# Performance work log

Hardware: AMD Instinct MI355X
Metric: run time of the kernel (lower is better)

## Reference

```python
import jax, jax.numpy as jnp
import numpy as np

N_NODES = 32768
N_EDGES = 524288
HID = 128


def _linear_params(key, fan_in, fan_out):
    kw, kb = jax.random.split(key)
    bound = 1.0 / np.sqrt(fan_in)
    w = jax.random.uniform(kw, (fan_in, fan_out), jnp.float32, -bound, bound)
    b = jax.random.uniform(kb, (fan_out,), jnp.float32, -bound, bound)
    return w, b


def setup_inputs() -> dict:
    key = jax.random.key(0)
    ks = jax.random.split(key, 8)
    x = jax.random.normal(ks[0], (N_NODES, HID), jnp.float32)
    edge_attr = jax.random.normal(ks[1], (N_EDGES, HID), jnp.float32)
    edges = jax.random.randint(ks[2], (2, N_EDGES), 0, N_NODES, jnp.int32)
    w1, b1 = _linear_params(ks[3], 3 * HID, HID)      # message_fn layer 1
    w2, b2 = _linear_params(ks[4], HID, HID)          # message_fn layer 2
    wu1, bu1 = _linear_params(ks[5], HID, 2 * HID)    # update_fn layer 1
    wu2, bu2 = _linear_params(ks[6], 2 * HID, HID)    # update_fn layer 2
    return {"x": x, "edge_attr": edge_attr, "edges": edges,
            "w1": w1, "b1": b1, "w2": w2, "b2": b2,
            "wu1": wu1, "bu1": bu1, "wu2": wu2, "bu2": bu2}


def reference(x, edge_attr, edges, w1, b1, w2, b2, wu1, bu1, wu2, bu2):
    n_nodes = x.shape[0]
    send, recv = edges[0], edges[1]
    # gather endpoint features and concat with edge attributes: [E, 3*HID]
    ea = jnp.concatenate([x[send], x[recv], edge_attr], axis=-1)
    # per-edge message MLP (Linear-SiLU-Linear-SiLU)
    h = jax.nn.silu(ea @ w1 + b1)
    msg = jax.nn.silu(h @ w2 + b2)                    # [E, HID]
    # scatter-mean into receiving nodes
    sums = jax.ops.segment_sum(msg, recv, num_segments=n_nodes)
    counts = jax.ops.segment_sum(jnp.ones((msg.shape[0],), msg.dtype), recv,
                                 num_segments=n_nodes)
    aggr = sums / jnp.maximum(counts, 1.0)[:, None]
    # residual (input_size == hidden_size -> Identity) + update MLP
    xo = x + aggr
    xo = xo + (jax.nn.silu(xo @ wu1 + bu1) @ wu2 + bu2)
    return xo, msg
```

## Files before the change

### kernel.cpp

```cpp
#include <hip/hip_runtime.h>
#include <hip/hip_bf16.h>

#define NN 32768
#define NE 524288
#define HID 128

typedef unsigned short u16;
typedef unsigned int u32;
typedef __bf16 bf16x8 __attribute__((ext_vector_type(8)));
typedef float f32x4 __attribute__((ext_vector_type(4)));

__device__ __forceinline__ u16 f2bf(float f) {
  return __builtin_bit_cast(u16, (__bf16)f);
}
__device__ __forceinline__ float silu_f(float v) {
  return v * __builtin_amdgcn_rcpf(1.f + __expf(-v));
}
__device__ __forceinline__ bf16x8 cvt8(float4 a, float4 b) {
  bf16x8 r;
  r[0] = (__bf16)a.x; r[1] = (__bf16)a.y; r[2] = (__bf16)a.z; r[3] = (__bf16)a.w;
  r[4] = (__bf16)b.x; r[5] = (__bf16)b.y; r[6] = (__bf16)b.z; r[7] = (__bf16)b.w;
  return r;
}
__device__ __forceinline__ float4 f4fma(float4 x, float4 s, float inv) {
  return make_float4(x.x + s.x * inv, x.y + s.y * inv,
                     x.z + s.z * inv, x.w + s.w * inv);
}

__device__ __forceinline__ void gld16(const void* g, void* l) {
  __builtin_amdgcn_global_load_lds(
      (const __attribute__((address_space(1))) u32*)g,
      (__attribute__((address_space(3))) u32*)l, 16, 0, 0);
}

#define WV(N)  do { asm volatile("s_waitcnt vmcnt(" #N ")" ::: "memory"); \
                    __builtin_amdgcn_sched_barrier(0); } while (0)
#define WVL(N) do { asm volatile("s_waitcnt vmcnt(" #N ") lgkmcnt(0)" ::: "memory"); \
                    __builtin_amdgcn_sched_barrier(0); } while (0)
#define WL()   do { asm volatile("s_waitcnt lgkmcnt(0)" ::: "memory"); \
                    __builtin_amdgcn_sched_barrier(0); } while (0)
__device__ __forceinline__ void bar() {
  __builtin_amdgcn_sched_barrier(0);
  __builtin_amdgcn_s_barrier();
  __builtin_amdgcn_sched_barrier(0);
}

__global__ __launch_bounds__(256) void prep_k(
    const float* __restrict__ x, const float* __restrict__ w1,
    const float* __restrict__ w2, const float* __restrict__ wu1,
    const float* __restrict__ wu2, const int* __restrict__ recv,
    u16* __restrict__ xb, u16* __restrict__ w1Ts, u16* __restrict__ w2Ts,
    u16* __restrict__ wu1T, u16* __restrict__ wu2T, int* __restrict__ cnt)
{
  int i = blockIdx.x * 256 + threadIdx.x;
  xb[i] = f2bf(x[i]);
  if (i < NE) atomicAdd(&cnt[recv[i]], 1);
  if (i < 3 * 128 * 128) {
    int j = i & 7, qs = (i >> 3) & 15, c = (i >> 7) & 127, s = i >> 14;
    int k = s * 128 + ((qs ^ (c & 7)) << 3) + j;
    w1Ts[i] = f2bf(w1[k * 128 + c]);
  }
  if (i < 128 * 128) {
    int j = i & 7, qs = (i >> 3) & 15, c = i >> 7;
    int k = ((qs ^ (c & 7)) << 3) + j;
    w2Ts[i] = f2bf(w2[k * 128 + c]);
  }
  if (i < 256 * 128) { int c = i >> 7, k = i & 127; wu1T[i] = f2bf(wu1[k * 256 + c]); }
  if (i < 128 * 256) { int c = i >> 8, k = i & 255; wu2T[i] = f2bf(wu2[k * 128 + c]); }
}

__global__ __launch_bounds__(1024) void scan_k(const int* __restrict__ cnt,
                                               int* __restrict__ cursor)
{
  __shared__ int part[1024];
  const int tid = threadIdx.x;
  const int base = tid * 32;
  int v[32];
  int s = 0;
  #pragma unroll
  for (int j = 0; j < 32; ++j) { v[j] = cnt[base + j]; s += v[j]; }
  part[tid] = s;
  __syncthreads();
  #pragma unroll 1
  for (int d = 1; d < 1024; d <<= 1) {
    int t = (tid >= d) ? part[tid - d] : 0;
    __syncthreads();
    part[tid] += t;
    __syncthreads();
  }
  int ex = part[tid] - s;
  #pragma unroll
  for (int j = 0; j < 32; ++j) {
    cursor[base + j] = ex;
    ex += v[j];
  }
}

__global__ __launch_bounds__(256) void scatter_k(const int* __restrict__ recv,
                                                 int* __restrict__ cursor,
                                                 int* __restrict__ eperm)
{
  int e = blockIdx.x * 256 + threadIdx.x;
  int r = recv[e];
  int pos = atomicAdd(&cursor[r], 1);
  eperm[pos] = e;
}

__global__ __launch_bounds__(512, 4) void edge_mlp(
    const u16* __restrict__ xb, const float* __restrict__ eattr,
    const int* __restrict__ send, const int* __restrict__ recv,
    const int* __restrict__ eperm,
    const u16* __restrict__ w1Ts, const float* __restrict__ b1,
    const u16* __restrict__ w2Ts, const float* __restrict__ b2,
    float* __restrict__ msg_out, float* __restrict__ sums)
{
  __shared__ u16 sA[128 * 128];
  __shared__ u16 sB[128 * 128];
  __shared__ int sNid[128];

  const int tid  = threadIdx.x;
  const int lane = tid & 63;
  const int w    = tid >> 6;
  const int wr   = w >> 1;
  const int wc   = w & 1;
  const int fr   = lane & 15;
  const int fkq  = lane >> 4;
  const int orow = fkq * 4;
  const int lrow4 = lane >> 4;
  const int schk  = lane & 15;
  const int logical = ((int)blockIdx.x & 7) * ((int)gridDim.x >> 3)
                    + ((int)blockIdx.x >> 3);
  const int e0 = logical * 128;

  int eo[4], ns[4], nr[4], rl[4];
  #pragma unroll
  for (int i = 0; i < 4; ++i) {
    rl[i] = w * 16 + i * 4 + lrow4;
    eo[i] = eperm[e0 + rl[i]];
  }
  #pragma unroll
  for (int i = 0; i < 4; ++i) {
    ns[i] = send[eo[i]];
    nr[i] = recv[eo[i]];
    if (schk == 0) sNid[rl[i]] = nr[i];
  }

  f32x4 acc[2][4];
  #pragma unroll
  for (int m = 0; m < 2; ++m)
    #pragma unroll
    for (int n = 0; n < 4; ++n)
      #pragma unroll
      for (int r = 0; r < 4; ++r) acc[m][n][r] = 0.f;

  #pragma unroll
  for (int i = 0; i < 4; ++i)
    gld16(xb + ((size_t)ns[i] << 7) + ((schk ^ (rl[i] & 7)) << 3),
          sA + ((w * 16 + i * 4) << 7));
  #pragma unroll
  for (int i = 0; i < 4; ++i)
    gld16(w1Ts + ((w * 16 + i * 4) << 7) + (lane << 3),
          sB + ((w * 16 + i * 4) << 7));
  __builtin_amdgcn_sched_barrier(0);
  float4 ea0[4], ea1[4];
  #pragma unroll
  for (int i = 0; i < 4; ++i) {
    const float* ep = eattr + ((size_t)eo[i] << 7) + ((schk ^ (rl[i] & 7)) << 3);
    ea0[i] = *reinterpret_cast<const float4*>(ep);
    ea1[i] = *reinterpret_cast<const float4*>(ep + 4);
  }
  __builtin_amdgcn_sched_barrier(0);

  auto cslice = [&](const u16* bufA) {
    #pragma unroll
    for (int kk = 0; kk < 4; ++kk) {
      bf16x8 aF[2], bF[4];
      #pragma unroll
      for (int m = 0; m < 2; ++m) {
        int row = wr * 32 + m * 16 + fr;
        int ch = (kk * 4 + fkq) ^ (row & 7);
        aF[m] = __builtin_bit_cast(bf16x8,
            *reinterpret_cast<const uint4*>(bufA + (row << 7) + (ch << 3)));
      }
      #pragma unroll
      for (int n = 0; n < 4; ++n) {
        int c = wc * 64 + n * 16 + fr;
        int ch = (kk * 4 + fkq) ^ (c & 7);
        bF[n] = __builtin_bit_cast(bf16x8,
            *reinterpret_cast<const uint4*>(sB + (c << 7) + (ch << 3)));
      }
      __builtin_amdgcn_s_setprio(1);
      #pragma unroll
      for (int m = 0; m < 2; ++m)
        #pragma unroll
        for (int n = 0; n < 4; ++n)
          acc[m][n] = __builtin_amdgcn_mfma_f32_16x16x32_bf16(aF[m], bF[n], acc[m][n], 0, 0, 0);
      __builtin_amdgcn_s_setprio(0);
    }
  };

  WV(8); bar();
  float b1v[4], b2v[4];
  #pragma unroll
  for (int n = 0; n < 4; ++n) {
    b1v[n] = b1[wc * 64 + n * 16 + fr];
    b2v[n] = b2[wc * 64 + n * 16 + fr];
  }
  cslice(sA);
  bar();
  #pragma unroll
  for (int i = 0; i < 4; ++i)
    gld16(xb + ((size_t)nr[i] << 7) + ((schk ^ (rl[i] & 7)) << 3),
          sA + ((w * 16 + i * 4) << 7));
  #pragma unroll
  for (int i = 0; i < 4; ++i)
    gld16(w1Ts + 16384 + ((w * 16 + i * 4) << 7) + (lane << 3),
          sB + ((w * 16 + i * 4) << 7));
  WV(0); bar();
  cslice(sA);
  bar();
  #pragma unroll
  for (int i = 0; i < 4; ++i)
    *reinterpret_cast<uint4*>(sA + (rl[i] << 7) + (schk << 3)) =
        __builtin_bit_cast(uint4, cvt8(ea0[i], ea1[i]));
  #pragma unroll
  for (int i = 0; i < 4; ++i)
    gld16(w1Ts + 32768 + ((w * 16 + i * 4) << 7) + (lane << 3),
          sB + ((w * 16 + i * 4) << 7));
  WVL(0); bar();
  cslice(sA);
  bar();
  #pragma unroll
  for (int i = 0; i < 4; ++i)
    gld16(w2Ts + ((w * 16 + i * 4) << 7) + (lane << 3),
          sB + ((w * 16 + i * 4) << 7));
  #pragma unroll
  for (int n = 0; n < 4; ++n) {
    int c = wc * 64 + n * 16 + fr;
    #pragma unroll
    for (int m = 0; m < 2; ++m)
      #pragma unroll
      for (int r = 0; r < 4; ++r) {
        int row = wr * 32 + m * 16 + orow + r;
        sA[(row << 7) + (((c >> 3) ^ (row & 7)) << 3) + (c & 7)] =
            f2bf(silu_f(acc[m][n][r] + b1v[n]));
        acc[m][n][r] = 0.f;
      }
  }
  WVL(0); bar();
  cslice(sA);

  int eg0[4], eg1[4];
  #pragma unroll
  for (int r = 0; r < 4; ++r) {
    eg0[r] = eperm[e0 + wr * 32 + orow + r];
    eg1[r] = eperm[e0 + wr * 32 + 16 + orow + r];
  }
  bar();

  #pragma unroll
  for (int m = 0; m < 2; ++m)
    #pragma unroll
    for (int r = 0; r < 4; ++r) {
      int row = wr * 32 + m * 16 + orow + r;
      float* mp = msg_out + ((size_t)(m ? eg1[r] : eg0[r]) << 7);
      #pragma unroll
      for (int n = 0; n < 4; ++n) {
        int c = wc * 64 + n * 16 + fr;
        float v = silu_f(acc[m][n][r] + b2v[n]);
        mp[c] = v;
        sA[(row << 7) + (((c >> 3) ^ (row & 7)) << 3) + (c & 7)] = f2bf(v);
      }
    }
  WL(); bar();

  {
    const int col = tid & 127, q = tid >> 7;
    float s = 0.f;
    int cur = sNid[q * 32];
    #pragma unroll 1
    for (int r = 0; r < 32; ++r) {
      int row = q * 32 + r;
      u16 hv = sA[(row << 7) + (((col >> 3) ^ (row & 7)) << 3) + (col & 7)];
      s += __builtin_bit_cast(float, (u32)hv << 16);
      int nxt = (r < 31) ? sNid[row + 1] : -1;
      if (nxt != cur) {
        atomicAdd(sums + (size_t)cur * HID + col, s);
        s = 0.f;
        cur = nxt;
      }
    }
  }
}

__global__ __launch_bounds__(256) void mlp1_k(
    const float* __restrict__ x, const float* __restrict__ sums,
    const int* __restrict__ cnt, const u16* __restrict__ wu1T,
    const float* __restrict__ bu1, u16* __restrict__ t)
{
  __shared__ u16 sB[256][40];
  const int tid = threadIdx.x, lane = tid & 63, wid = tid >> 6;
  const int wr = wid >> 1, wc = wid & 1;
  const int fr = lane & 15, fkq = lane >> 4, fk = fkq * 8, orow = fkq * 4;
  const int n0 = blockIdx.x * 64;

  float invm[2];
  #pragma unroll
  for (int m = 0; m < 2; ++m)
    invm[m] = __builtin_amdgcn_rcpf(fmaxf((float)cnt[n0 + wr * 32 + m * 16 + fr], 1.f));

  f32x4 acc[2][8];
  #pragma unroll
  for (int m = 0; m < 2; ++m)
    #pragma unroll
    for (int n = 0; n < 8; ++n)
      #pragma unroll
      for (int r = 0; r < 4; ++r) acc[m][n][r] = 0.f;

  #pragma unroll 1
  for (int kk = 0; kk < 4; ++kk) {
    #pragma unroll
    for (int it = 0; it < 4; ++it) {
      int chunk = tid + it * 256;
      int c = chunk >> 2, q = chunk & 3;
      *reinterpret_cast<uint4*>(&sB[c][q * 8]) =
          *reinterpret_cast<const uint4*>(wu1T + c * 128 + kk * 32 + q * 8);
    }
    __syncthreads();
    bf16x8 aF[2], bF[8];
    #pragma unroll
    for (int m = 0; m < 2; ++m) {
      size_t base = (size_t)(n0 + wr * 32 + m * 16 + fr) * HID + kk * 32 + fk;
      float4 xv0 = *reinterpret_cast<const float4*>(x + base);
      float4 xv1 = *reinterpret_cast<const float4*>(x + base + 4);
      float4 sv0 = *reinterpret_cast<const float4*>(sums + base);
      float4 sv1 = *reinterpret_cast<const float4*>(sums + base + 4);
      aF[m] = cvt8(f4fma(xv0, sv0, invm[m]), f4fma(xv1, sv1, invm[m]));
    }
    #pragma unroll
    for (int n = 0; n < 8; ++n)
      bF[n] = __builtin_bit_cast(bf16x8,
          *reinterpret_cast<const uint4*>(&sB[wc * 128 + n * 16 + fr][fk]));
    #pragma unroll
    for (int m = 0; m < 2; ++m)
      #pragma unroll
      for (int n = 0; n < 8; ++n)
        acc[m][n] = __builtin_amdgcn_mfma_f32_16x16x32_bf16(aF[m], bF[n], acc[m][n], 0, 0, 0);
    __syncthreads();
  }
  #pragma unroll
  for (int n = 0; n < 8; ++n) {
    int col = wc * 128 + n * 16 + fr;
    float bb = bu1[col];
    #pragma unroll
    for (int m = 0; m < 2; ++m) {
      int row = n0 + wr * 32 + m * 16 + orow;
      #pragma unroll
      for (int r = 0; r < 4; ++r)
        t[(size_t)(row + r) * 256 + col] = f2bf(silu_f(acc[m][n][r] + bb));
    }
  }
}

__global__ __launch_bounds__(256) void mlp2_k(
    const u16* __restrict__ t, const u16* __restrict__ wu2T,
    const float* __restrict__ bu2, const float* __restrict__ x,
    const float* __restrict__ sums, const int* __restrict__ cnt,
    float* __restrict__ xo)
{
  __shared__ u16 sB[128][40];
  const int tid = threadIdx.x, lane = tid & 63, wid = tid >> 6;
  const int wr = wid >> 1, wc = wid & 1;
  const int fr = lane & 15, fk = (lane >> 4) * 8, orow = (lane >> 4) * 4;
  const int n0 = blockIdx.x * 64;

  f32x4 acc[2][4];
  #pragma unroll
  for (int m = 0; m < 2; ++m)
    #pragma unroll
    for (int n = 0; n < 4; ++n)
      #pragma unroll
      for (int r = 0; r < 4; ++r) acc[m][n][r] = 0.f;

  #pragma unroll 1
  for (int kk = 0; kk < 8; ++kk) {
    #pragma unroll
    for (int it = 0; it < 2; ++it) {
      int chunk = tid + it * 256;
      int c = chunk >> 2, q = chunk & 3;
      *reinterpret_cast<uint4*>(&sB[c][q * 8]) =
          *reinterpret_cast<const uint4*>(wu2T + c * 256 + kk * 32 + q * 8);
    }
    __syncthreads();
    bf16x8 aF[2], bF[4];
    #pragma unroll
    for (int m = 0; m < 2; ++m)
      aF[m] = __builtin_bit_cast(bf16x8, *reinterpret_cast<const uint4*>(
          t + (size_t)(n0 + wr * 32 + m * 16 + fr) * 256 + kk * 32 + fk));
    #pragma unroll
    for (int n = 0; n < 4; ++n)
      bF[n] = __builtin_bit_cast(bf16x8,
          *reinterpret_cast<const uint4*>(&sB[wc * 64 + n * 16 + fr][fk]));
    #pragma unroll
    for (int m = 0; m < 2; ++m)
      #pragma unroll
      for (int n = 0; n < 4; ++n)
        acc[m][n] = __builtin_amdgcn_mfma_f32_16x16x32_bf16(aF[m], bF[n], acc[m][n], 0, 0, 0);
    __syncthreads();
  }
  #pragma unroll
  for (int m = 0; m < 2; ++m) {
    #pragma unroll
    for (int r = 0; r < 4; ++r) {
      int gn = n0 + wr * 32 + m * 16 + orow + r;
      float inv = 1.f / fmaxf((float)cnt[gn], 1.f);
      #pragma unroll
      for (int n = 0; n < 4; ++n) {
        int col = wc * 64 + n * 16 + fr;
        float xi = x[(size_t)gn * HID + col] + sums[(size_t)gn * HID + col] * inv;
        xo[(size_t)gn * HID + col] = xi + acc[m][n][r] + bu2[col];
      }
    }
  }
}

extern "C" void kernel_launch(void* const* d_in, const int* in_sizes, int n_in,
                              void* d_out, int out_size, void* d_ws, size_t ws_size,
                              hipStream_t stream)
{
  (void)in_sizes; (void)n_in; (void)out_size; (void)ws_size;
  const float* x     = (const float*)d_in[0];
  const float* eattr = (const float*)d_in[1];
  const int*   edges = (const int*)d_in[2];
  const float* w1  = (const float*)d_in[3];
  const float* b1  = (const float*)d_in[4];
  const float* w2  = (const float*)d_in[5];
  const float* b2  = (const float*)d_in[6];
  const float* wu1 = (const float*)d_in[7];
  const float* bu1 = (const float*)d_in[8];
  const float* wu2 = (const float*)d_in[9];
  const float* bu2 = (const float*)d_in[10];

  float* xo  = (float*)d_out;
  float* msg = xo + (size_t)NN * HID;

  char* p = (char*)d_ws;
  u16* xb    = (u16*)p; p += (size_t)NN * HID * 2;
  u16* w1Ts  = (u16*)p; p += 384 * 128 * 2;
  u16* w2Ts  = (u16*)p; p += 128 * 128 * 2;
  u16* wu1T  = (u16*)p; p += 256 * 128 * 2;
  u16* wu2T  = (u16*)p; p += 128 * 256 * 2;
  u16* tbuf  = (u16*)p; p += (size_t)NN * 256 * 2;
  float* sums = (float*)p; p += (size_t)NN * HID * 4;
  int* cnt    = (int*)p; p += (size_t)NN * 4;
  int* cursor = (int*)p; p += (size_t)NN * 4;
  int* eperm  = (int*)p; p += (size_t)NE * 4;

  const int* send = edges;
  const int* recv = edges + NE;

  hipMemsetAsync(cnt, 0, (size_t)NN * 4, stream);
  hipMemsetAsync(sums, 0, (size_t)NN * HID * 4, stream);
  prep_k<<<NN * HID / 256, 256, 0, stream>>>(x, w1, w2, wu1, wu2, recv,
                                             xb, w1Ts, w2Ts, wu1T, wu2T, cnt);
  scan_k<<<1, 1024, 0, stream>>>(cnt, cursor);
  scatter_k<<<NE / 256, 256, 0, stream>>>(recv, cursor, eperm);
  edge_mlp<<<NE / 128, 512, 0, stream>>>(xb, eattr, send, recv, eperm,
                                         w1Ts, b1, w2Ts, b2, msg, sums);
  mlp1_k<<<NN / 64, 256, 0, stream>>>(x, sums, cnt, wu1T, bu1, tbuf);
  mlp2_k<<<NN / 64, 256, 0, stream>>>(tbuf, wu2T, bu2, x, sums, cnt, xo);
}
```

Before: 324.5 us.

## Halve edge tile to 64 rows with separate sender/receiver LDS buffers

Shrinks the edge_mlp tile from 128 to 64 edges per block and rearranges the 8 waves as 2x4 over the output tile, with each wave computing a 32x32 slice. Sender and receiver node gathers go into two separate LDS buffers, so both are issued up front instead of the receiver gather waiting until after the first K-slice. This is meant to lower LDS use and register pressure, raising occupancy, and to overlap the gather latency. In exchange the full weight tiles are loaded into LDS twice as often in total and the block count doubles.

```diff
diff --git a/kernel.cpp b/kernel.cpp
--- a/kernel.cpp
+++ b/kernel.cpp
@@ -34,8 +34,6 @@
 }
 
 #define WV(N)  do { asm volatile("s_waitcnt vmcnt(" #N ")" ::: "memory"); \
-                    __builtin_amdgcn_sched_barrier(0); } while (0)
-#define WVL(N) do { asm volatile("s_waitcnt vmcnt(" #N ") lgkmcnt(0)" ::: "memory"); \
                     __builtin_amdgcn_sched_barrier(0); } while (0)
 #define WL()   do { asm volatile("s_waitcnt lgkmcnt(0)" ::: "memory"); \
                     __builtin_amdgcn_sched_barrier(0); } while (0)
@@ -114,15 +112,16 @@
     const u16* __restrict__ w2Ts, const float* __restrict__ b2,
     float* __restrict__ msg_out, float* __restrict__ sums)
 {
-  __shared__ u16 sA[128 * 128];
-  __shared__ u16 sB[128 * 128];
-  __shared__ int sNid[128];
+  __shared__ u16 sA0[64 * 128];
+  __shared__ u16 sA1[64 * 128];
+  __shared__ u16 sB[128 * 128 / 2 * 2];
+  __shared__ int sNid[64];
 
   const int tid  = threadIdx.x;
   const int lane = tid & 63;
   const int w    = tid >> 6;
-  const int wr   = w >> 1;
-  const int wc   = w & 1;
+  const int wr   = w >> 2;
+  const int wc   = w & 3;
   const int fr   = lane & 15;
   const int fkq  = lane >> 4;
   const int orow = fkq * 4;
@@ -130,51 +129,63 @@
   const int schk  = lane & 15;
   const int logical = ((int)blockIdx.x & 7) * ((int)gridDim.x >> 3)
                     + ((int)blockIdx.x >> 3);
-  const int e0 = logical * 128;
-
-  int eo[4], ns[4], nr[4], rl[4];
-  #pragma unroll
-  for (int i = 0; i < 4; ++i) {
-    rl[i] = w * 16 + i * 4 + lrow4;
+  const int e0 = logical * 64;
+
+  int eo[2], ns[2], nr[2], rl[2];
+  #pragma unroll
+  for (int i = 0; i < 2; ++i) {
+    rl[i] = w * 8 + i * 4 + lrow4;
     eo[i] = eperm[e0 + rl[i]];
   }
   #pragma unroll
-  for (int i = 0; i < 4; ++i) {
+  for (int i = 0; i < 2; ++i) {
     ns[i] = send[eo[i]];
     nr[i] = recv[eo[i]];
     if (schk == 0) sNid[rl[i]] = nr[i];
   }
 
-  f32x4 acc[2][4];
-  #pragma unroll
-  for (int m = 0; m < 2; ++m)
-    #pragma unroll
-    for (int n = 0; n < 4; ++n)
+  f32x4 acc[2][2];
+  #pragma unroll
+  for (int m = 0; m < 2; ++m)
+    #pragma unroll
+    for (int n = 0; n < 2; ++n)
       #pragma unroll
       for (int r = 0; r < 4; ++r) acc[m][n][r] = 0.f;
 
-  #pragma unroll
-  for (int i = 0; i < 4; ++i)
+  float b1v[2], b2v[2];
+  #pragma unroll
+  for (int n = 0; n < 2; ++n) {
+    b1v[n] = b1[wc * 32 + n * 16 + fr];
+    b2v[n] = b2[wc * 32 + n * 16 + fr];
+  }
+  __builtin_amdgcn_sched_barrier(0);
+  #pragma unroll
+  for (int i = 0; i < 2; ++i)
     gld16(xb + ((size_t)ns[i] << 7) + ((schk ^ (rl[i] & 7)) << 3),
-          sA + ((w * 16 + i * 4) << 7));
+          sA0 + ((w * 8 + i * 4) << 7));
   #pragma unroll
   for (int i = 0; i < 4; ++i)
     gld16(w1Ts + ((w * 16 + i * 4) << 7) + (lane << 3),
           sB + ((w * 16 + i * 4) << 7));
   __builtin_amdgcn_sched_barrier(0);
-  float4 ea0[4], ea1[4];
-  #pragma unroll
-  for (int i = 0; i < 4; ++i) {
+  #pragma unroll
+  for (int i = 0; i < 2; ++i)
+    gld16(xb + ((size_t)nr[i] << 7) + ((schk ^ (rl[i] & 7)) << 3),
+          sA1 + ((w * 8 + i * 4) << 7));
+  __builtin_amdgcn_sched_barrier(0);
+  float4 ea[2][2];
+  #pragma unroll
+  for (int i = 0; i < 2; ++i) {
     const float* ep = eattr + ((size_t)eo[i] << 7) + ((schk ^ (rl[i] & 7)) << 3);
-    ea0[i] = *reinterpret_cast<const float4*>(ep);
-    ea1[i] = *reinterpret_cast<const float4*>(ep + 4);
+    ea[i][0] = *reinterpret_cast<const float4*>(ep);
+    ea[i][1] = *reinterpret_cast<const float4*>(ep + 4);
   }
   __builtin_amdgcn_sched_barrier(0);
 
   auto cslice = [&](const u16* bufA) {
     #pragma unroll
     for (int kk = 0; kk < 4; ++kk) {
-      bf16x8 aF[2], bF[4];
+      bf16x8 aF[2], bF[2];
       #pragma unroll
       for (int m = 0; m < 2; ++m) {
         int row = wr * 32 + m * 16 + fr;
@@ -183,8 +194,8 @@
             *reinterpret_cast<const uint4*>(bufA + (row << 7) + (ch << 3)));
       }
       #pragma unroll
-      for (int n = 0; n < 4; ++n) {
-        int c = wc * 64 + n * 16 + fr;
+      for (int n = 0; n < 2; ++n) {
+        int c = wc * 32 + n * 16 + fr;
         int ch = (kk * 4 + fkq) ^ (c & 7);
         bF[n] = __builtin_bit_cast(bf16x8,
             *reinterpret_cast<const uint4*>(sB + (c << 7) + (ch << 3)));
@@ -193,69 +204,58 @@
       #pragma unroll
       for (int m = 0; m < 2; ++m)
         #pragma unroll
-        for (int n = 0; n < 4; ++n)
+        for (int n = 0; n < 2; ++n)
           acc[m][n] = __builtin_amdgcn_mfma_f32_16x16x32_bf16(aF[m], bF[n], acc[m][n], 0, 0, 0);
       __builtin_amdgcn_s_setprio(0);
     }
   };
 
-  WV(8); bar();
-  float b1v[4], b2v[4];
-  #pragma unroll
-  for (int n = 0; n < 4; ++n) {
-    b1v[n] = b1[wc * 64 + n * 16 + fr];
-    b2v[n] = b2[wc * 64 + n * 16 + fr];
-  }
-  cslice(sA);
+  WV(6); bar();
+  cslice(sA0);
   bar();
-  #pragma unroll
-  for (int i = 0; i < 4; ++i)
-    gld16(xb + ((size_t)nr[i] << 7) + ((schk ^ (rl[i] & 7)) << 3),
-          sA + ((w * 16 + i * 4) << 7));
   #pragma unroll
   for (int i = 0; i < 4; ++i)
     gld16(w1Ts + 16384 + ((w * 16 + i * 4) << 7) + (lane << 3),
           sB + ((w * 16 + i * 4) << 7));
   WV(0); bar();
-  cslice(sA);
+  cslice(sA1);
   bar();
   #pragma unroll
-  for (int i = 0; i < 4; ++i)
-    *reinterpret_cast<uint4*>(sA + (rl[i] << 7) + (schk << 3)) =
-        __builtin_bit_cast(uint4, cvt8(ea0[i], ea1[i]));
+  for (int i = 0; i < 2; ++i)
+    *reinterpret_cast<uint4*>(sA0 + (rl[i] << 7) + (schk << 3)) =
+        __builtin_bit_cast(uint4, cvt8(ea[i][0], ea[i][1]));
   #pragma unroll
   for (int i = 0; i < 4; ++i)
     gld16(w1Ts + 32768 + ((w * 16 + i * 4) << 7) + (lane << 3),
           sB + ((w * 16 + i * 4) << 7));
-  WVL(0); bar();
-  cslice(sA);
+  WV(0); WL(); bar();
+  cslice(sA0);
   bar();
   #pragma unroll
   for (int i = 0; i < 4; ++i)
     gld16(w2Ts + ((w * 16 + i * 4) << 7) + (lane << 3),
           sB + ((w * 16 + i * 4) << 7));
   #pragma unroll
-  for (int n = 0; n < 4; ++n) {
-    int c = wc * 64 + n * 16 + fr;
-    #pragma unroll
-    for (int m = 0; m < 2; ++m)
+  for (int m = 0; m < 2; ++m)
+    #pragma unroll
+    for (int n = 0; n < 2; ++n) {
+      int c = wc * 32 + n * 16 + fr;
       #pragma unroll
       for (int r = 0; r < 4; ++r) {
         int row = wr * 32 + m * 16 + orow + r;
-        sA[(row << 7) + (((c >> 3) ^ (row & 7)) << 3) + (c & 7)] =
+        sA1[(row << 7) + (((c >> 3) ^ (row & 7)) << 3) + (c & 7)] =
             f2bf(silu_f(acc[m][n][r] + b1v[n]));
         acc[m][n][r] = 0.f;
       }
-  }
-  WVL(0); bar();
-  cslice(sA);
-
-  int eg0[4], eg1[4];
-  #pragma unroll
-  for (int r = 0; r < 4; ++r) {
-    eg0[r] = eperm[e0 + wr * 32 + orow + r];
-    eg1[r] = eperm[e0 + wr * 32 + 16 + orow + r];
-  }
+    }
+  WV(0); WL(); bar();
+  int eg[2][4];
+  #pragma unroll
+  for (int m = 0; m < 2; ++m)
+    #pragma unroll
+    for (int r = 0; r < 4; ++r)
+      eg[m][r] = eperm[e0 + wr * 32 + m * 16 + orow + r];
+  cslice(sA1);
   bar();
 
   #pragma unroll
@@ -263,13 +263,13 @@
     #pragma unroll
     for (int r = 0; r < 4; ++r) {
       int row = wr * 32 + m * 16 + orow + r;
-      float* mp = msg_out + ((size_t)(m ? eg1[r] : eg0[r]) << 7);
-      #pragma unroll
-      for (int n = 0; n < 4; ++n) {
-        int c = wc * 64 + n * 16 + fr;
+      float* mp = msg_out + ((size_t)eg[m][r] << 7);
+      #pragma unroll
+      for (int n = 0; n < 2; ++n) {
+        int c = wc * 32 + n * 16 + fr;
         float v = silu_f(acc[m][n][r] + b2v[n]);
         mp[c] = v;
-        sA[(row << 7) + (((c >> 3) ^ (row & 7)) << 3) + (c & 7)] = f2bf(v);
+        sA0[(row << 7) + (((c >> 3) ^ (row & 7)) << 3) + (c & 7)] = f2bf(v);
       }
     }
   WL(); bar();
@@ -277,13 +277,13 @@
   {
     const int col = tid & 127, q = tid >> 7;
     float s = 0.f;
-    int cur = sNid[q * 32];
+    int cur = sNid[q * 16];
     #pragma unroll 1
-    for (int r = 0; r < 32; ++r) {
-      int row = q * 32 + r;
-      u16 hv = sA[(row << 7) + (((col >> 3) ^ (row & 7)) << 3) + (col & 7)];
+    for (int r = 0; r < 16; ++r) {
+      int row = q * 16 + r;
+      u16 hv = sA0[(row << 7) + (((col >> 3) ^ (row & 7)) << 3) + (col & 7)];
       s += __builtin_bit_cast(float, (u32)hv << 16);
-      int nxt = (r < 31) ? sNid[row + 1] : -1;
+      int nxt = (r < 15) ? sNid[row + 1] : -1;
       if (nxt != cur) {
         atomicAdd(sums + (size_t)cur * HID + col, s);
         s = 0.f;
@@ -465,8 +465,8 @@
                                              xb, w1Ts, w2Ts, wu1T, wu2T, cnt);
   scan_k<<<1, 1024, 0, stream>>>(cnt, cursor);
   scatter_k<<<NE / 256, 256, 0, stream>>>(recv, cursor, eperm);
-  edge_mlp<<<NE / 128, 512, 0, stream>>>(xb, eattr, send, recv, eperm,
-                                         w1Ts, b1, w2Ts, b2, msg, sums);
+  edge_mlp<<<NE / 64, 512, 0, stream>>>(xb, eattr, send, recv, eperm,
+                                        w1Ts, b1, w2Ts, b2, msg, sums);
   mlp1_k<<<NN / 64, 256, 0, stream>>>(x, sums, cnt, wu1T, bu1, tbuf);
   mlp2_k<<<NN / 64, 256, 0, stream>>>(tbuf, wu2T, bu2, x, sums, cnt, xo);
 }
```

Result: no change. 327.1 us (+0.8%).

## Halve edge-MLP weight LDS staging, pre-permute endpoint ids, vectorize x conversion

Applied to the files above, without the earlier changes.

The edge MLP now stages each 128-column weight panel into shared memory as two 64-column halves. This cuts LDS use so the launch bound can rise to 6 blocks per CU, at the cost of twice as many barrier-separated stage and compute steps. The scatter kernel now also writes sender and receiver ids in sorted order, so the edge MLP no longer makes dependent indirect loads through eperm to fetch them. The edge-attribute prefetch is moved later and loses its overlap with the first GEMM slices. Separately, prep_k converts x to bf16 four floats per thread, so it launches a quarter as many blocks.

```diff
diff --git a/kernel.cpp b/kernel.cpp
--- a/kernel.cpp
+++ b/kernel.cpp
@@ -12,6 +12,9 @@
 
 __device__ __forceinline__ u16 f2bf(float f) {
   return __builtin_bit_cast(u16, (__bf16)f);
+}
+__device__ __forceinline__ float bf2f(u16 h) {
+  return __builtin_bit_cast(float, (u32)h << 16);
 }
 __device__ __forceinline__ float silu_f(float v) {
   return v * __builtin_amdgcn_rcpf(1.f + __expf(-v));
@@ -34,8 +37,6 @@
 }
 
 #define WV(N)  do { asm volatile("s_waitcnt vmcnt(" #N ")" ::: "memory"); \
-                    __builtin_amdgcn_sched_barrier(0); } while (0)
-#define WVL(N) do { asm volatile("s_waitcnt vmcnt(" #N ") lgkmcnt(0)" ::: "memory"); \
                     __builtin_amdgcn_sched_barrier(0); } while (0)
 #define WL()   do { asm volatile("s_waitcnt lgkmcnt(0)" ::: "memory"); \
                     __builtin_amdgcn_sched_barrier(0); } while (0)
@@ -53,7 +54,11 @@
     u16* __restrict__ wu1T, u16* __restrict__ wu2T, int* __restrict__ cnt)
 {
   int i = blockIdx.x * 256 + threadIdx.x;
-  xb[i] = f2bf(x[i]);
+  float4 xv = reinterpret_cast<const float4*>(x)[i];
+  uint2 pv;
+  pv.x = (u32)f2bf(xv.x) | ((u32)f2bf(xv.y) << 16);
+  pv.y = (u32)f2bf(xv.z) | ((u32)f2bf(xv.w) << 16);
+  reinterpret_cast<uint2*>(xb)[i] = pv;
   if (i < NE) atomicAdd(&cnt[recv[i]], 1);
   if (i < 3 * 128 * 128) {
     int j = i & 7, qs = (i >> 3) & 15, c = (i >> 7) & 127, s = i >> 14;
@@ -96,26 +101,32 @@
   }
 }
 
-__global__ __launch_bounds__(256) void scatter_k(const int* __restrict__ recv,
+__global__ __launch_bounds__(256) void scatter_k(const int* __restrict__ send,
+                                                 const int* __restrict__ recv,
                                                  int* __restrict__ cursor,
-                                                 int* __restrict__ eperm)
+                                                 int* __restrict__ eperm,
+                                                 int* __restrict__ sid,
+                                                 int* __restrict__ rid)
 {
   int e = blockIdx.x * 256 + threadIdx.x;
   int r = recv[e];
+  int s = send[e];
   int pos = atomicAdd(&cursor[r], 1);
   eperm[pos] = e;
-}
-
-__global__ __launch_bounds__(512, 4) void edge_mlp(
+  sid[pos] = s;
+  rid[pos] = r;
+}
+
+__global__ __launch_bounds__(512, 6) void edge_mlp(
     const u16* __restrict__ xb, const float* __restrict__ eattr,
-    const int* __restrict__ send, const int* __restrict__ recv,
-    const int* __restrict__ eperm,
-    const u16* __restrict__ w1Ts, const float* __restrict__ b1,
-    const u16* __restrict__ w2Ts, const float* __restrict__ b2,
+    const int* __restrict__ eperm, const int* __restrict__ sid,
+    const int* __restrict__ rid,
+    const u16* __restrict__ wTs, const float* __restrict__ b1,
+    const float* __restrict__ b2,
     float* __restrict__ msg_out, float* __restrict__ sums)
 {
   __shared__ u16 sA[128 * 128];
-  __shared__ u16 sB[128 * 128];
+  __shared__ u16 sB[64 * 128];
   __shared__ int sNid[128];
 
   const int tid  = threadIdx.x;
@@ -137,125 +148,128 @@
   for (int i = 0; i < 4; ++i) {
     rl[i] = w * 16 + i * 4 + lrow4;
     eo[i] = eperm[e0 + rl[i]];
-  }
-  #pragma unroll
-  for (int i = 0; i < 4; ++i) {
-    ns[i] = send[eo[i]];
-    nr[i] = recv[eo[i]];
+    ns[i] = sid[e0 + rl[i]];
+    nr[i] = rid[e0 + rl[i]];
+  }
+  #pragma unroll
+  for (int i = 0; i < 4; ++i)
     if (schk == 0) sNid[rl[i]] = nr[i];
-  }
-
-  f32x4 acc[2][4];
-  #pragma unroll
-  for (int m = 0; m < 2; ++m)
-    #pragma unroll
-    for (int n = 0; n < 4; ++n)
-      #pragma unroll
-      for (int r = 0; r < 4; ++r) acc[m][n][r] = 0.f;
-
-  #pragma unroll
-  for (int i = 0; i < 4; ++i)
-    gld16(xb + ((size_t)ns[i] << 7) + ((schk ^ (rl[i] & 7)) << 3),
-          sA + ((w * 16 + i * 4) << 7));
-  #pragma unroll
-  for (int i = 0; i < 4; ++i)
-    gld16(w1Ts + ((w * 16 + i * 4) << 7) + (lane << 3),
-          sB + ((w * 16 + i * 4) << 7));
-  __builtin_amdgcn_sched_barrier(0);
-  float4 ea0[4], ea1[4];
-  #pragma unroll
-  for (int i = 0; i < 4; ++i) {
-    const float* ep = eattr + ((size_t)eo[i] << 7) + ((schk ^ (rl[i] & 7)) << 3);
-    ea0[i] = *reinterpret_cast<const float4*>(ep);
-    ea1[i] = *reinterpret_cast<const float4*>(ep + 4);
-  }
-  __builtin_amdgcn_sched_barrier(0);
-
-  auto cslice = [&](const u16* bufA) {
+
+  float b1v[2][2], b2v[2][2];
+  #pragma unroll
+  for (int h = 0; h < 2; ++h)
+    #pragma unroll
+    for (int n = 0; n < 2; ++n) {
+      int c = h * 64 + wc * 32 + n * 16 + fr;
+      b1v[h][n] = b1[c];
+      b2v[h][n] = b2[c];
+    }
+
+  f32x4 acc[2][2][2];
+  #pragma unroll
+  for (int h = 0; h < 2; ++h)
+    #pragma unroll
+    for (int m = 0; m < 2; ++m)
+      #pragma unroll
+      for (int n = 0; n < 2; ++n)
+        #pragma unroll
+        for (int r = 0; r < 4; ++r) acc[h][m][n][r] = 0.f;
+
+  auto stageA = [&](const int (&node)[4]) {
+    #pragma unroll
+    for (int i = 0; i < 4; ++i)
+      gld16(xb + ((size_t)node[i] << 7) + ((schk ^ (rl[i] & 7)) << 3),
+            sA + ((w * 16 + i * 4) << 7));
+  };
+  auto stageB = [&](int panel, int h) {
+    const u16* src = wTs + panel * 16384 + h * 8192;
+    gld16(src + (w * 2 + 0) * 512 + lane * 8, sB + (w * 2 + 0) * 512);
+    gld16(src + (w * 2 + 1) * 512 + lane * 8, sB + (w * 2 + 1) * 512);
+  };
+
+  auto chalf = [&](f32x4 (&a)[2][2]) {
     #pragma unroll
     for (int kk = 0; kk < 4; ++kk) {
-      bf16x8 aF[2], bF[4];
+      bf16x8 aF[2], bF[2];
       #pragma unroll
       for (int m = 0; m < 2; ++m) {
         int row = wr * 32 + m * 16 + fr;
         int ch = (kk * 4 + fkq) ^ (row & 7);
         aF[m] = __builtin_bit_cast(bf16x8,
-            *reinterpret_cast<const uint4*>(bufA + (row << 7) + (ch << 3)));
+            *reinterpret_cast<const uint4*>(sA + (row << 7) + (ch << 3)));
       }
       #pragma unroll
-      for (int n = 0; n < 4; ++n) {
-        int c = wc * 64 + n * 16 + fr;
-        int ch = (kk * 4 + fkq) ^ (c & 7);
+      for (int n = 0; n < 2; ++n) {
+        int cl = wc * 32 + n * 16 + fr;
+        int ch = (kk * 4 + fkq) ^ (cl & 7);
         bF[n] = __builtin_bit_cast(bf16x8,
-            *reinterpret_cast<const uint4*>(sB + (c << 7) + (ch << 3)));
+            *reinterpret_cast<const uint4*>(sB + (cl << 7) + (ch << 3)));
       }
       __builtin_amdgcn_s_setprio(1);
       #pragma unroll
       for (int m = 0; m < 2; ++m)
         #pragma unroll
-        for (int n = 0; n < 4; ++n)
-          acc[m][n] = __builtin_amdgcn_mfma_f32_16x16x32_bf16(aF[m], bF[n], acc[m][n], 0, 0, 0);
+        for (int n = 0; n < 2; ++n)
+          a[m][n] = __builtin_amdgcn_mfma_f32_16x16x32_bf16(aF[m], bF[n], a[m][n], 0, 0, 0);
       __builtin_amdgcn_s_setprio(0);
     }
   };
 
-  WV(8); bar();
-  float b1v[4], b2v[4];
-  #pragma unroll
-  for (int n = 0; n < 4; ++n) {
-    b1v[n] = b1[wc * 64 + n * 16 + fr];
-    b2v[n] = b2[wc * 64 + n * 16 + fr];
-  }
-  cslice(sA);
-  bar();
-  #pragma unroll
-  for (int i = 0; i < 4; ++i)
-    gld16(xb + ((size_t)nr[i] << 7) + ((schk ^ (rl[i] & 7)) << 3),
-          sA + ((w * 16 + i * 4) << 7));
-  #pragma unroll
-  for (int i = 0; i < 4; ++i)
-    gld16(w1Ts + 16384 + ((w * 16 + i * 4) << 7) + (lane << 3),
-          sB + ((w * 16 + i * 4) << 7));
+  stageA(ns);
+  stageB(0, 0);
   WV(0); bar();
-  cslice(sA);
-  bar();
-  #pragma unroll
-  for (int i = 0; i < 4; ++i)
+  chalf(acc[0]); bar();
+  stageB(0, 1); WV(0); bar();
+  chalf(acc[1]); bar();
+
+  stageA(nr);
+  stageB(1, 0);
+  WV(0); bar();
+  chalf(acc[0]); bar();
+  stageB(1, 1); WV(0); bar();
+  chalf(acc[1]); bar();
+
+  stageB(2, 0);
+  #pragma unroll
+  for (int i = 0; i < 4; ++i) {
+    const float* ep = eattr + ((size_t)eo[i] << 7) + ((schk ^ (rl[i] & 7)) << 3);
+    float4 v0 = *reinterpret_cast<const float4*>(ep);
+    float4 v1 = *reinterpret_cast<const float4*>(ep + 4);
     *reinterpret_cast<uint4*>(sA + (rl[i] << 7) + (schk << 3)) =
-        __builtin_bit_cast(uint4, cvt8(ea0[i], ea1[i]));
-  #pragma unroll
-  for (int i = 0; i < 4; ++i)
-    gld16(w1Ts + 32768 + ((w * 16 + i * 4) << 7) + (lane << 3),
-          sB + ((w * 16 + i * 4) << 7));
-  WVL(0); bar();
-  cslice(sA);
-  bar();
-  #pragma unroll
-  for (int i = 0; i < 4; ++i)
-    gld16(w2Ts + ((w * 16 + i * 4) << 7) + (lane << 3),
-          sB + ((w * 16 + i * 4) << 7));
-  #pragma unroll
-  for (int n = 0; n < 4; ++n) {
-    int c = wc * 64 + n * 16 + fr;
+        __builtin_bit_cast(uint4, cvt8(v0, v1));
+  }
+  WV(0); WL(); bar();
+  chalf(acc[0]); bar();
+  stageB(2, 1); WV(0); bar();
+  chalf(acc[1]); bar();
+
+  stageB(3, 0);
+  #pragma unroll
+  for (int h = 0; h < 2; ++h)
     #pragma unroll
     for (int m = 0; m < 2; ++m)
       #pragma unroll
-      for (int r = 0; r < 4; ++r) {
-        int row = wr * 32 + m * 16 + orow + r;
-        sA[(row << 7) + (((c >> 3) ^ (row & 7)) << 3) + (c & 7)] =
-            f2bf(silu_f(acc[m][n][r] + b1v[n]));
-        acc[m][n][r] = 0.f;
+      for (int n = 0; n < 2; ++n) {
+        int c = h * 64 + wc * 32 + n * 16 + fr;
+        #pragma unroll
+        for (int r = 0; r < 4; ++r) {
+          int row = wr * 32 + m * 16 + orow + r;
+          sA[(row << 7) + (((c >> 3) ^ (row & 7)) << 3) + (c & 7)] =
+              f2bf(silu_f(acc[h][m][n][r] + b1v[h][n]));
+          acc[h][m][n][r] = 0.f;
+        }
       }
-  }
-  WVL(0); bar();
-  cslice(sA);
-
-  int eg0[4], eg1[4];
-  #pragma unroll
-  for (int r = 0; r < 4; ++r) {
-    eg0[r] = eperm[e0 + wr * 32 + orow + r];
-    eg1[r] = eperm[e0 + wr * 32 + 16 + orow + r];
-  }
+  WV(0); WL(); bar();
+  chalf(acc[0]); bar();
+  stageB(3, 1); WV(0); bar();
+  chalf(acc[1]);
+
+  int eg[2][4];
+  #pragma unroll
+  for (int m = 0; m < 2; ++m)
+    #pragma unroll
+    for (int r = 0; r < 4; ++r)
+      eg[m][r] = eperm[e0 + wr * 32 + m * 16 + orow + r];
   bar();
 
   #pragma unroll
@@ -263,14 +277,16 @@
     #pragma unroll
     for (int r = 0; r < 4; ++r) {
       int row = wr * 32 + m * 16 + orow + r;
-      float* mp = msg_out + ((size_t)(m ? eg1[r] : eg0[r]) << 7);
-      #pragma unroll
-      for (int n = 0; n < 4; ++n) {
-        int c = wc * 64 + n * 16 + fr;
-        float v = silu_f(acc[m][n][r] + b2v[n]);
-        mp[c] = v;
-        sA[(row << 7) + (((c >> 3) ^ (row & 7)) << 3) + (c & 7)] = f2bf(v);
-      }
+      float* mp = msg_out + ((size_t)eg[m][r] << 7);
+      #pragma unroll
+      for (int h = 0; h < 2; ++h)
+        #pragma unroll
+        for (int n = 0; n < 2; ++n) {
+          int c = h * 64 + wc * 32 + n * 16 + fr;
+          float v = silu_f(acc[h][m][n][r] + b2v[h][n]);
+          mp[c] = v;
+          sA[(row << 7) + (((c >> 3) ^ (row & 7)) << 3) + (c & 7)] = f2bf(v);
+        }
     }
   WL(); bar();
 
@@ -282,7 +298,7 @@
     for (int r = 0; r < 32; ++r) {
       int row = q * 32 + r;
       u16 hv = sA[(row << 7) + (((col >> 3) ^ (row & 7)) << 3) + (col & 7)];
-      s += __builtin_bit_cast(float, (u32)hv << 16);
+      s += bf2f(hv);
       int nxt = (r < 31) ? sNid[row + 1] : -1;
       if (nxt != cur) {
         atomicAdd(sums + (size_t)cur * HID + col, s);
@@ -330,11 +346,11 @@
     bf16x8 aF[2], bF[8];
     #pragma unroll
     for (int m = 0; m < 2; ++m) {
-      size_t base = (size_t)(n0 + wr * 32 + m * 16 + fr) * HID + kk * 32 + fk;
-      float4 xv0 = *reinterpret_cast<const float4*>(x + base);
-      float4 xv1 = *reinterpret_cast<const float4*>(x + base + 4);
-      float4 sv0 = *reinterpret_cast<const float4*>(sums + base);
-      float4 sv1 = *reinterpret_cast<const float4*>(sums + base + 4);
+      size_t basei = (size_t)(n0 + wr * 32 + m * 16 + fr) * HID + kk * 32 + fk;
+      float4 xv0 = *reinterpret_cast<const float4*>(x + basei);
+      float4 xv1 = *reinterpret_cast<const float4*>(x + basei + 4);
+      float4 sv0 = *reinterpret_cast<const float4*>(sums + basei);
+      float4 sv1 = *reinterpret_cast<const float4*>(sums + basei + 4);
       aF[m] = cvt8(f4fma(xv0, sv0, invm[m]), f4fma(xv1, sv1, invm[m]));
     }
     #pragma unroll
@@ -455,18 +471,20 @@
   int* cnt    = (int*)p; p += (size_t)NN * 4;
   int* cursor = (int*)p; p += (size_t)NN * 4;
   int* eperm  = (int*)p; p += (size_t)NE * 4;
+  int* sid    = (int*)p; p += (size_t)NE * 4;
+  int* rid    = (int*)p; p += (size_t)NE * 4;
 
   const int* send = edges;
   const int* recv = edges + NE;
 
   hipMemsetAsync(cnt, 0, (size_t)NN * 4, stream);
   hipMemsetAsync(sums, 0, (size_t)NN * HID * 4, stream);
-  prep_k<<<NN * HID / 256, 256, 0, stream>>>(x, w1, w2, wu1, wu2, recv,
-                                             xb, w1Ts, w2Ts, wu1T, wu2T, cnt);
+  prep_k<<<NN * HID / 4 / 256, 256, 0, stream>>>(x, w1, w2, wu1, wu2, recv,
+                                                 xb, w1Ts, w2Ts, wu1T, wu2T, cnt);
   scan_k<<<1, 1024, 0, stream>>>(cnt, cursor);
-  scatter_k<<<NE / 256, 256, 0, stream>>>(recv, cursor, eperm);
-  edge_mlp<<<NE / 128, 512, 0, stream>>>(xb, eattr, send, recv, eperm,
-                                         w1Ts, b1, w2Ts, b2, msg, sums);
+  scatter_k<<<NE / 256, 256, 0, stream>>>(send, recv, cursor, eperm, sid, rid);
+  edge_mlp<<<NE / 128, 512, 0, stream>>>(xb, eattr, eperm, sid, rid,
+                                         w1Ts, b1, b2, msg, sums);
   mlp1_k<<<NN / 64, 256, 0, stream>>>(x, sums, cnt, wu1T, bu1, tbuf);
   mlp2_k<<<NN / 64, 256, 0, stream>>>(tbuf, wu2T, bu2, x, sums, cnt, xo);
 }
```

New measurement: 385.3 us. 1.19x slower.
